# Performance work log

Hardware: AMD Instinct MI355X
Metric: run time of the kernel (lower is better)

The kernel has to match this reference:

```python
import jax, jax.numpy as jnp
import numpy as np
from jax import lax

N = 100000   # nodes
E = 3200000  # edges
D = 10       # feature dim (input_dim == output_dim == 10)
H = 16       # hidden dim of gnn1


def setup_inputs() -> dict:
    key = jax.random.key(0)
    ks = jax.random.split(key, 12)
    def g(k, shape, scale=0.1):
        return jax.random.normal(k, shape, jnp.float32) * scale
    return {
        "x": jax.random.normal(ks[0], (N, D), jnp.float32),
        "edge_index": jax.random.randint(ks[1], (2, E), 0, N, dtype=jnp.int32),
        "W1": g(ks[2], (D, H)),   # gnn1 weight
        "b1": jnp.zeros((H,), jnp.float32),
        "W2": g(ks[3], (H, D)),   # gnn2 weight
        "b2": jnp.zeros((D,), jnp.float32),
        "cW1": g(ks[4], (16, 1, 3)),   # Conv1d(1,16,3) OIH
        "cb1": jnp.zeros((16,), jnp.float32),
        "cW2": g(ks[5], (32, 16, 3)),  # Conv1d(16,32,3) OIH
        "cb2": jnp.zeros((32,), jnp.float32),
        "Wout": g(ks[6], (64, 2)),     # Linear(64, 2)
        "bout": jnp.zeros((2,), jnp.float32),
    }


def gcn_conv(x, src, dst, W, b, n):
    h = x @ W                                       # [N, F_out]
    loop = jnp.arange(n, dtype=src.dtype)
    s = jnp.concatenate([src, loop])
    d = jnp.concatenate([dst, loop])
    deg = jax.ops.segment_sum(jnp.ones(s.shape, h.dtype), d, num_segments=n)
    dinv = lax.rsqrt(jnp.maximum(deg, 1e-12))
    norm = dinv[s] * dinv[d]                        # [E+N]
    msg = h[s] * norm[:, None]                      # gather + scale
    out = jax.ops.segment_sum(msg, d, num_segments=n)  # scatter-add
    return out + b


def conv_block(x, W, b):
    # Conv1d(k=3, stride=1, pad=1) + ReLU + MaxPool1d(2)
    y = lax.conv_general_dilated(x, W, (1,), [(1, 1)],
                                 dimension_numbers=("NCH", "OIH", "NCH"))
    y = jax.nn.relu(y + b[None, :, None])
    return lax.reduce_window(y, -jnp.inf, lax.max, (1, 1, 2), (1, 1, 2), "VALID")


def reference(x, edge_index, W1, b1, W2, b2, cW1, cb1, cW2, cb2, Wout, bout):
    src, dst = edge_index[0], edge_index[1]
    n = x.shape[0]
    x_g = jax.nn.relu(gcn_conv(x, src, dst, W1, b1, n))
    # F.dropout with training=False is identity (eval mode)
    x_g = gcn_conv(x_g, src, dst, W2, b2, n)
    x_dual = x + x_g                                # residual add
    y = x_dual[:, None, :]                          # [N, 1, 10]
    y = conv_block(y, cW1, cb1)                     # [N, 16, 5]
    y = conv_block(y, cW2, cb2)                     # [N, 32, 2]
    y = y.reshape(n, -1)                            # [N, 64]
    out = y @ Wout + bout                           # [N, 2]
    return jax.nn.softmax(out, axis=1)
```

## Files before the change

### kernel.cpp

```cpp
#include <hip/hip_runtime.h>
#include <hip/hip_fp16.h>
#include <math.h>

#define TPB 256
#define TPB_P 512
#define NB_E 256
#define NPB 256
#define NBKT_CAP 512
#define BKT_CAP 8960

__global__ void histA_kernel(const int* __restrict__ ei, int E, int chunk, int nbkt,
                             int* __restrict__ counts) {
    __shared__ int h[NBKT_CAP];
    for (int b = threadIdx.x; b < NBKT_CAP; b += TPB_P) h[b] = 0;
    __syncthreads();
    int beg = blockIdx.x * chunk;
    int end = beg + chunk; if (end > E) end = E;
    for (int k = beg + threadIdx.x; k < end; k += TPB_P)
        atomicAdd(&h[ei[E + k] >> 8], 1);
    __syncthreads();
    for (int b = threadIdx.x; b < nbkt; b += TPB_P)
        counts[(size_t)b * NB_E + blockIdx.x] = h[b];
}

__global__ void scanB1_kernel(int* __restrict__ counts, int* __restrict__ totals) {
    int b = blockIdx.x, tid = threadIdx.x;
    int c = counts[(size_t)b * NB_E + tid];
    __shared__ int sc[TPB];
    sc[tid] = c;
    __syncthreads();
    for (int off = 1; off < TPB; off <<= 1) {
        int v = (tid >= off) ? sc[tid - off] : 0;
        __syncthreads();
        sc[tid] += v;
        __syncthreads();
    }
    counts[(size_t)b * NB_E + tid] = sc[tid] - c;
    if (tid == TPB - 1) totals[b] = sc[tid];
}

__global__ void scanB2_kernel(const int* __restrict__ totals, int* __restrict__ base, int nbkt) {
    __shared__ int s[NBKT_CAP];
    int t = threadIdx.x;
    int v0 = (t < nbkt) ? totals[t] : 0;
    s[t] = v0;
    __syncthreads();
    for (int off = 1; off < NBKT_CAP; off <<= 1) {
        int v = (t >= off) ? s[t - off] : 0;
        __syncthreads();
        s[t] += v;
        __syncthreads();
    }
    if (t < nbkt) {
        base[t] = s[t] - v0;
        if (t == nbkt - 1) base[nbkt] = s[t];
    }
}

__global__ void placeC_kernel(const int* __restrict__ ei, int E, int chunk, int nbkt,
                              const int* __restrict__ offs, const int* __restrict__ base,
                              unsigned* __restrict__ pairs) {
    __shared__ int lcur[NBKT_CAP];
    for (int b = threadIdx.x; b < nbkt; b += TPB_P)
        lcur[b] = offs[(size_t)b * NB_E + blockIdx.x] + base[b];
    __syncthreads();
    int beg = blockIdx.x * chunk;
    int end = beg + chunk; if (end > E) end = E;
    for (int k = beg + threadIdx.x; k < end; k += TPB_P) {
        int s = ei[k];
        int d = ei[E + k];
        int pos = atomicAdd(&lcur[d >> 8], 1);
        pairs[pos] = ((unsigned)s << 8) | (unsigned)(d & 255);
    }
}

__global__ __launch_bounds__(TPB) void sortD_kernel(unsigned* __restrict__ pairs,
                                                    const int* __restrict__ base, int N, int E,
                                                    int* __restrict__ rowstart,
                                                    float* __restrict__ dinv,
                                                    const float* __restrict__ x,
                                                    const float* __restrict__ W1,
                                                    __half* __restrict__ g1h) {
    __shared__ unsigned sp[BKT_CAP];
    __shared__ int lh[NPB];
    __shared__ int lsc[NPB];
    __shared__ int lcur[NPB];
    __shared__ float sW1[160];
    int b = blockIdx.x, beg = base[b], end = base[b + 1];
    int cnt = end - beg;
    if (cnt > BKT_CAP) cnt = BKT_CAP;
    if (threadIdx.x < 160) sW1[threadIdx.x] = W1[threadIdx.x];
    for (int k = threadIdx.x; k < cnt; k += TPB) sp[k] = pairs[beg + k];
    lh[threadIdx.x] = 0;
    __syncthreads();
    for (int k = threadIdx.x; k < cnt; k += TPB) atomicAdd(&lh[sp[k] & 255], 1);
    __syncthreads();
    int myh = lh[threadIdx.x];
    lsc[threadIdx.x] = myh;
    __syncthreads();
    for (int off = 1; off < NPB; off <<= 1) {
        int v = (threadIdx.x >= off) ? lsc[threadIdx.x - off] : 0;
        __syncthreads();
        lsc[threadIdx.x] += v;
        __syncthreads();
    }
    int excl = lsc[threadIdx.x] - myh;
    lcur[threadIdx.x] = excl;
    int v = b * NPB + threadIdx.x;
    float dv = rsqrtf((float)myh + 1.0f);
    if (v < N) {
        rowstart[v] = beg + excl;
        dinv[v] = dv;
        if (v == N - 1) rowstart[N] = E;
    }
    __syncthreads();
    for (int k = threadIdx.x; k < cnt; k += TPB) {
        unsigned p = sp[k];
        int pos = atomicAdd(&lcur[p & 255], 1);
        pairs[beg + pos] = p >> 8;
    }
    if (v < N) {
        float xv[10];
#pragma unroll
        for (int i = 0; i < 10; ++i) xv[i] = x[(size_t)v * 10 + i];
        float o[16];
#pragma unroll
        for (int j = 0; j < 16; ++j) {
            float h = 0.f;
#pragma unroll
            for (int i = 0; i < 10; ++i) h = fmaf(xv[i], sW1[i * 16 + j], h);
            o[j] = h * dv;
        }
        unsigned u[8];
#pragma unroll
        for (int q = 0; q < 8; ++q) {
            __half2 hh = __floats2half2_rn(o[2 * q], o[2 * q + 1]);
            u[q] = *reinterpret_cast<unsigned*>(&hh);
        }
        uint4* gp = (uint4*)(g1h + (size_t)v * 16);
        gp[0] = make_uint4(u[0], u[1], u[2], u[3]);
        gp[1] = make_uint4(u[4], u[5], u[6], u[7]);
    }
}

__global__ void gatherA_kernel(const int* __restrict__ rowstart, const unsigned* __restrict__ srcs,
                               const __half2* __restrict__ g1h, const float* __restrict__ dinv,
                               const float* __restrict__ b1, const float* __restrict__ W2,
                               __half* __restrict__ g2h, int N) {
    __shared__ float sxg[32][17];
    __shared__ float sdinv[32];
    __shared__ float sW2[160];
    __shared__ float sb1[16];
    if (threadIdx.x < 160) sW2[threadIdx.x] = W2[threadIdx.x];
    if (threadIdx.x < 16) sb1[threadIdx.x] = b1[threadIdx.x];
    int l = threadIdx.x >> 3;
    int j = threadIdx.x & 7;
    int v = blockIdx.x * 32 + l;
    if (v < N) {
        int beg = rowstart[v], end = rowstart[v + 1];
        float2 f = __half22float2(g1h[(size_t)v * 8 + j]);
        float ax = f.x, ay = f.y;
        int k = beg;
        int n4 = beg + ((end - beg) & ~3);
        for (; k < n4; k += 4) {
            unsigned s0 = srcs[k], s1 = srcs[k + 1], s2 = srcs[k + 2], s3 = srcs[k + 3];
            float2 f0 = __half22float2(g1h[(size_t)s0 * 8 + j]);
            float2 f1 = __half22float2(g1h[(size_t)s1 * 8 + j]);
            float2 f2 = __half22float2(g1h[(size_t)s2 * 8 + j]);
            float2 f3 = __half22float2(g1h[(size_t)s3 * 8 + j]);
            ax += (f0.x + f1.x) + (f2.x + f3.x);
            ay += (f0.y + f1.y) + (f2.y + f3.y);
        }
        for (; k < end; ++k) {
            float2 fe = __half22float2(g1h[(size_t)srcs[k] * 8 + j]);
            ax += fe.x; ay += fe.y;
        }
        float dv = dinv[v];
        sxg[l][2 * j]     = fmaxf(fmaf(dv, ax, sb1[2 * j]), 0.f);
        sxg[l][2 * j + 1] = fmaxf(fmaf(dv, ay, sb1[2 * j + 1]), 0.f);
        if (j == 0) sdinv[l] = dv;
    }
    __syncthreads();
    for (int idx = threadIdx.x; idx < 320; idx += TPB) {
        int l2 = idx / 10, i = idx % 10;
        int v2 = blockIdx.x * 32 + l2;
        if (v2 < N) {
            float acc = 0.f;
#pragma unroll
            for (int jj = 0; jj < 16; ++jj) acc = fmaf(sxg[l2][jj], sW2[jj * 10 + i], acc);
            g2h[(size_t)v2 * 10 + i] = __float2half(acc * sdinv[l2]);
        }
    }
}

__global__ void gather10_kernel(const int* __restrict__ rowstart, const unsigned* __restrict__ srcs,
                                const __half* __restrict__ g2h, float* __restrict__ acc2, int N) {
    int t = blockIdx.x * blockDim.x + threadIdx.x;
    int v = t / 10;
    int j = t % 10;
    if (v >= N) return;
    int beg = rowstart[v], end = rowstart[v + 1];
    float acc = __half2float(g2h[(size_t)v * 10 + j]);
    int k = beg;
    int n4 = beg + ((end - beg) & ~3);
    for (; k < n4; k += 4) {
        unsigned s0 = srcs[k], s1 = srcs[k + 1], s2 = srcs[k + 2], s3 = srcs[k + 3];
        float a0 = __half2float(g2h[(size_t)s0 * 10 + j]);
        float a1 = __half2float(g2h[(size_t)s1 * 10 + j]);
        float a2 = __half2float(g2h[(size_t)s2 * 10 + j]);
        float a3 = __half2float(g2h[(size_t)s3 * 10 + j]);
        acc += (a0 + a1) + (a2 + a3);
    }
    for (; k < end; ++k) acc += __half2float(g2h[(size_t)srcs[k] * 10 + j]);
    acc2[(size_t)v * 10 + j] = acc;
}

__global__ void final_kernel(const float* __restrict__ x, const float* __restrict__ acc2,
                             const float* __restrict__ dinv, const float* __restrict__ b2,
                             const float* __restrict__ cW1, const float* __restrict__ cb1,
                             const float* __restrict__ cW2, const float* __restrict__ cb2,
                             const float* __restrict__ Wout, const float* __restrict__ bout,
                             float* __restrict__ out, int N) {
    __shared__ float s_cW1[48];
    __shared__ float s_cb1[16];
    __shared__ float s_cW2[1536];
    __shared__ float s_cb2[32];
    __shared__ float s_Wout[128];
    __shared__ float s_bout[2];
    for (int i = threadIdx.x; i < 48; i += blockDim.x) s_cW1[i] = cW1[i];
    for (int i = threadIdx.x; i < 16; i += blockDim.x) s_cb1[i] = cb1[i];
    for (int i = threadIdx.x; i < 1536; i += blockDim.x) s_cW2[i] = cW2[i];
    for (int i = threadIdx.x; i < 32; i += blockDim.x) s_cb2[i] = cb2[i];
    for (int i = threadIdx.x; i < 128; i += blockDim.x) s_Wout[i] = Wout[i];
    if (threadIdx.x < 2) s_bout[threadIdx.x] = bout[threadIdx.x];
    __syncthreads();

    int v = blockIdx.x * blockDim.x + threadIdx.x;
    if (v >= N) return;
    float dv = dinv[v];

    float xd[12];
    xd[0] = 0.f;
    xd[11] = 0.f;
#pragma unroll
    for (int i = 0; i < 10; ++i)
        xd[i + 1] = x[(size_t)v * 10 + i] + fmaf(dv, acc2[(size_t)v * 10 + i], b2[i]);

    float p1[16][7];
#pragma unroll
    for (int c = 0; c < 16; ++c) {
        float w0 = s_cW1[c * 3 + 0], w1 = s_cW1[c * 3 + 1], w2 = s_cW1[c * 3 + 2];
        float bc = s_cb1[c];
        p1[c][0] = 0.f;
        p1[c][6] = 0.f;
#pragma unroll
        for (int jj = 0; jj < 5; ++jj) {
            float y0 = fmaxf(fmaf(w0, xd[2 * jj + 0], fmaf(w1, xd[2 * jj + 1], fmaf(w2, xd[2 * jj + 2], bc))), 0.f);
            float y1 = fmaxf(fmaf(w0, xd[2 * jj + 1], fmaf(w1, xd[2 * jj + 2], fmaf(w2, xd[2 * jj + 3], bc))), 0.f);
            p1[c][jj + 1] = fmaxf(y0, y1);
        }
    }

    float z0 = s_bout[0], z1 = s_bout[1];
#pragma unroll
    for (int o = 0; o < 32; ++o) {
        float y2[5];
#pragma unroll
        for (int i = 0; i < 5; ++i) y2[i] = s_cb2[o];
#pragma unroll
        for (int c = 0; c < 16; ++c) {
            float w0 = s_cW2[o * 48 + c * 3 + 0];
            float w1 = s_cW2[o * 48 + c * 3 + 1];
            float w2 = s_cW2[o * 48 + c * 3 + 2];
#pragma unroll
            for (int i = 0; i < 5; ++i)
                y2[i] = fmaf(w0, p1[c][i], fmaf(w1, p1[c][i + 1], fmaf(w2, p1[c][i + 2], y2[i])));
        }
        float p20 = fmaxf(fmaxf(y2[0], 0.f), fmaxf(y2[1], 0.f));
        float p21 = fmaxf(fmaxf(y2[2], 0.f), fmaxf(y2[3], 0.f));
        z0 = fmaf(p20, s_Wout[(o * 2 + 0) * 2 + 0], z0);
        z1 = fmaf(p20, s_Wout[(o * 2 + 0) * 2 + 1], z1);
        z0 = fmaf(p21, s_Wout[(o * 2 + 1) * 2 + 0], z0);
        z1 = fmaf(p21, s_Wout[(o * 2 + 1) * 2 + 1], z1);
    }

    float m = fmaxf(z0, z1);
    float e0 = expf(z0 - m), e1 = expf(z1 - m);
    float inv = 1.f / (e0 + e1);
    out[(size_t)v * 2 + 0] = e0 * inv;
    out[(size_t)v * 2 + 1] = e1 * inv;
}

extern "C" void kernel_launch(void* const* d_in, const int* in_sizes, int n_in,
                              void* d_out, int out_size, void* d_ws, size_t ws_size,
                              hipStream_t stream) {
    const float* x    = (const float*)d_in[0];
    const int*   ei   = (const int*)d_in[1];
    const float* W1   = (const float*)d_in[2];
    const float* b1   = (const float*)d_in[3];
    const float* W2   = (const float*)d_in[4];
    const float* b2   = (const float*)d_in[5];
    const float* cW1  = (const float*)d_in[6];
    const float* cb1  = (const float*)d_in[7];
    const float* cW2  = (const float*)d_in[8];
    const float* cb2  = (const float*)d_in[9];
    const float* Wout = (const float*)d_in[10];
    const float* bout = (const float*)d_in[11];
    float* out = (float*)d_out;

    int N = in_sizes[0] / 10;
    int E = in_sizes[1] / 2;
    int nbkt = (N + NPB - 1) / NPB;
    int chunk = (E + NB_E - 1) / NB_E;
    int nb = (N + TPB - 1) / TPB;

    char* p = (char*)d_ws;
    __half*   g1h    = (__half*)p;
    int*      counts = (int*)p;      p += sizeof(__half) * (size_t)16 * N;
    int*      totals = (int*)p;      p += sizeof(int) * NBKT_CAP;
    int*      base   = (int*)p;      p += sizeof(int) * (NBKT_CAP + 1);
    int*      rowstart = (int*)p;    p += sizeof(int) * (size_t)(N + 1);
    float*    dinv   = (float*)p;    p += sizeof(float) * (size_t)N;
    unsigned* pairs  = (unsigned*)p; p += sizeof(unsigned) * (size_t)E;
    __half*   g2h    = (__half*)p;   p += sizeof(__half) * (size_t)10 * N;
    float*    acc2   = (float*)p;    p += sizeof(float) * (size_t)10 * N;

    histA_kernel<<<NB_E, TPB_P, 0, stream>>>(ei, E, chunk, nbkt, counts);
    scanB1_kernel<<<nbkt, TPB, 0, stream>>>(counts, totals);
    scanB2_kernel<<<1, NBKT_CAP, 0, stream>>>(totals, base, nbkt);
    placeC_kernel<<<NB_E, TPB_P, 0, stream>>>(ei, E, chunk, nbkt, counts, base, pairs);
    sortD_kernel<<<nbkt, TPB, 0, stream>>>(pairs, base, N, E, rowstart, dinv, x, W1, g1h);

    int ga = (N + 31) / 32;
    gatherA_kernel<<<ga, TPB, 0, stream>>>(rowstart, pairs, (const __half2*)g1h, dinv, b1, W2, g2h, N);
    int gb = (int)(((size_t)N * 10 + TPB - 1) / TPB);
    gather10_kernel<<<gb, TPB, 0, stream>>>(rowstart, pairs, g2h, acc2, N);
    final_kernel<<<nb, TPB, 0, stream>>>(x, acc2, dinv, b2, cW1, cb1, cW2, cb2, Wout, bout, out, N);
}
```

Before: 141.4 us.

## Pad second-layer features to 16 halves and gather with half2 lanes

The second GCN aggregation now stores g2h padded to 16 halves per node, so each node's row is 32 bytes and is read as eight half2 lanes, mirroring the first-layer gather. Each thread now handles two features and each node gets one aligned row, instead of ten scalar half loads at odd strides. This trades some extra bytes of padded gather traffic for fewer, aligned load instructions. Separately, the histogram and placement kernels now use 128 blocks of 1024 threads instead of 256 blocks of 512, and the per-bucket scan is resized to match.

```diff
diff --git a/kernel.cpp b/kernel.cpp
--- a/kernel.cpp
+++ b/kernel.cpp
@@ -3,13 +3,13 @@
 #include <math.h>
 
 #define TPB 256
-#define TPB_P 512
-#define NB_E 256
+#define TPB_P 1024
+#define NB_E 128
 #define NPB 256
 #define NBKT_CAP 512
 #define BKT_CAP 8960
 
-__global__ void histA_kernel(const int* __restrict__ ei, int E, int chunk, int nbkt,
+__global__ __launch_bounds__(TPB_P) void histA_kernel(const int* __restrict__ ei, int E, int chunk, int nbkt,
                              int* __restrict__ counts) {
     __shared__ int h[NBKT_CAP];
     for (int b = threadIdx.x; b < NBKT_CAP; b += TPB_P) h[b] = 0;
@@ -26,17 +26,17 @@
 __global__ void scanB1_kernel(int* __restrict__ counts, int* __restrict__ totals) {
     int b = blockIdx.x, tid = threadIdx.x;
     int c = counts[(size_t)b * NB_E + tid];
-    __shared__ int sc[TPB];
+    __shared__ int sc[NB_E];
     sc[tid] = c;
     __syncthreads();
-    for (int off = 1; off < TPB; off <<= 1) {
+    for (int off = 1; off < NB_E; off <<= 1) {
         int v = (tid >= off) ? sc[tid - off] : 0;
         __syncthreads();
         sc[tid] += v;
         __syncthreads();
     }
     counts[(size_t)b * NB_E + tid] = sc[tid] - c;
-    if (tid == TPB - 1) totals[b] = sc[tid];
+    if (tid == NB_E - 1) totals[b] = sc[tid];
 }
 
 __global__ void scanB2_kernel(const int* __restrict__ totals, int* __restrict__ base, int nbkt) {
@@ -57,7 +57,7 @@
     }
 }
 
-__global__ void placeC_kernel(const int* __restrict__ ei, int E, int chunk, int nbkt,
+__global__ __launch_bounds__(TPB_P) void placeC_kernel(const int* __restrict__ ei, int E, int chunk, int nbkt,
                               const int* __restrict__ offs, const int* __restrict__ base,
                               unsigned* __restrict__ pairs) {
     __shared__ int lcur[NBKT_CAP];
@@ -181,38 +181,47 @@
         if (j == 0) sdinv[l] = dv;
     }
     __syncthreads();
-    for (int idx = threadIdx.x; idx < 320; idx += TPB) {
-        int l2 = idx / 10, i = idx % 10;
+    for (int idx = threadIdx.x; idx < 512; idx += TPB) {
+        int l2 = idx >> 4, i = idx & 15;
         int v2 = blockIdx.x * 32 + l2;
         if (v2 < N) {
-            float acc = 0.f;
-#pragma unroll
-            for (int jj = 0; jj < 16; ++jj) acc = fmaf(sxg[l2][jj], sW2[jj * 10 + i], acc);
-            g2h[(size_t)v2 * 10 + i] = __float2half(acc * sdinv[l2]);
-        }
-    }
-}
-
-__global__ void gather10_kernel(const int* __restrict__ rowstart, const unsigned* __restrict__ srcs,
-                                const __half* __restrict__ g2h, float* __restrict__ acc2, int N) {
-    int t = blockIdx.x * blockDim.x + threadIdx.x;
-    int v = t / 10;
-    int j = t % 10;
+            float val = 0.f;
+            if (i < 10) {
+                float acc = 0.f;
+#pragma unroll
+                for (int jj = 0; jj < 16; ++jj) acc = fmaf(sxg[l2][jj], sW2[jj * 10 + i], acc);
+                val = acc * sdinv[l2];
+            }
+            g2h[(size_t)v2 * 16 + i] = __float2half(val);
+        }
+    }
+}
+
+__global__ void gatherB_kernel(const int* __restrict__ rowstart, const unsigned* __restrict__ srcs,
+                               const __half2* __restrict__ g2h, float* __restrict__ acc2, int N) {
+    int l = threadIdx.x >> 3;
+    int j = threadIdx.x & 7;
+    int v = blockIdx.x * 32 + l;
     if (v >= N) return;
     int beg = rowstart[v], end = rowstart[v + 1];
-    float acc = __half2float(g2h[(size_t)v * 10 + j]);
+    float2 f = __half22float2(g2h[(size_t)v * 8 + j]);
+    float ax = f.x, ay = f.y;
     int k = beg;
     int n4 = beg + ((end - beg) & ~3);
     for (; k < n4; k += 4) {
         unsigned s0 = srcs[k], s1 = srcs[k + 1], s2 = srcs[k + 2], s3 = srcs[k + 3];
-        float a0 = __half2float(g2h[(size_t)s0 * 10 + j]);
-        float a1 = __half2float(g2h[(size_t)s1 * 10 + j]);
-        float a2 = __half2float(g2h[(size_t)s2 * 10 + j]);
-        float a3 = __half2float(g2h[(size_t)s3 * 10 + j]);
-        acc += (a0 + a1) + (a2 + a3);
-    }
-    for (; k < end; ++k) acc += __half2float(g2h[(size_t)srcs[k] * 10 + j]);
-    acc2[(size_t)v * 10 + j] = acc;
+        float2 f0 = __half22float2(g2h[(size_t)s0 * 8 + j]);
+        float2 f1 = __half22float2(g2h[(size_t)s1 * 8 + j]);
+        float2 f2 = __half22float2(g2h[(size_t)s2 * 8 + j]);
+        float2 f3 = __half22float2(g2h[(size_t)s3 * 8 + j]);
+        ax += (f0.x + f1.x) + (f2.x + f3.x);
+        ay += (f0.y + f1.y) + (f2.y + f3.y);
+    }
+    for (; k < end; ++k) {
+        float2 fe = __half22float2(g2h[(size_t)srcs[k] * 8 + j]);
+        ax += fe.x; ay += fe.y;
+    }
+    ((float2*)(acc2 + (size_t)v * 16))[j] = make_float2(ax, ay);
 }
 
 __global__ void final_kernel(const float* __restrict__ x, const float* __restrict__ acc2,
@@ -244,7 +253,7 @@
     xd[11] = 0.f;
 #pragma unroll
     for (int i = 0; i < 10; ++i)
-        xd[i + 1] = x[(size_t)v * 10 + i] + fmaf(dv, acc2[(size_t)v * 10 + i], b2[i]);
+        xd[i + 1] = x[(size_t)v * 10 + i] + fmaf(dv, acc2[(size_t)v * 16 + i], b2[i]);
 
     float p1[16][7];
 #pragma unroll
@@ -322,18 +331,17 @@
     int*      rowstart = (int*)p;    p += sizeof(int) * (size_t)(N + 1);
     float*    dinv   = (float*)p;    p += sizeof(float) * (size_t)N;
     unsigned* pairs  = (unsigned*)p; p += sizeof(unsigned) * (size_t)E;
-    __half*   g2h    = (__half*)p;   p += sizeof(__half) * (size_t)10 * N;
-    float*    acc2   = (float*)p;    p += sizeof(float) * (size_t)10 * N;
+    __half*   g2h    = (__half*)p;   p += sizeof(__half) * (size_t)16 * N;
+    float*    acc2   = (float*)p;    p += sizeof(float) * (size_t)16 * N;
 
     histA_kernel<<<NB_E, TPB_P, 0, stream>>>(ei, E, chunk, nbkt, counts);
-    scanB1_kernel<<<nbkt, TPB, 0, stream>>>(counts, totals);
+    scanB1_kernel<<<nbkt, NB_E, 0, stream>>>(counts, totals);
     scanB2_kernel<<<1, NBKT_CAP, 0, stream>>>(totals, base, nbkt);
     placeC_kernel<<<NB_E, TPB_P, 0, stream>>>(ei, E, chunk, nbkt, counts, base, pairs);
     sortD_kernel<<<nbkt, TPB, 0, stream>>>(pairs, base, N, E, rowstart, dinv, x, W1, g1h);
 
     int ga = (N + 31) / 32;
     gatherA_kernel<<<ga, TPB, 0, stream>>>(rowstart, pairs, (const __half2*)g1h, dinv, b1, W2, g2h, N);
-    int gb = (int)(((size_t)N * 10 + TPB - 1) / TPB);
-    gather10_kernel<<<gb, TPB, 0, stream>>>(rowstart, pairs, g2h, acc2, N);
+    gatherB_kernel<<<ga, TPB, 0, stream>>>(rowstart, pairs, (const __half2*)g2h, acc2, N);
     final_kernel<<<nb, TPB, 0, stream>>>(x, acc2, dinv, b2, cW1, cb1, cW2, cb2, Wout, bout, out, N);
 }
```

After: 156.3 us. +10.5%, slower.
